# Kernel tuning notes

Measured on AMD Instinct MI355X. Metric: run time of the kernel, lower is better.

The kernel has to match this reference:

```python
import jax, jax.numpy as jnp
import numpy as np

H, C = 8, 16          # heads, per-head dim; hidden = H*C = 128
NEG_SLOPE = 0.2       # GATConv default
EPS = 1e-5            # GraphNorm eps


def setup_inputs() -> dict:
    key = jax.random.key(0)
    ks = iter(jax.random.split(key, 64))
    Np, Na, D, E = 100000, 50000, 128, 500000
    s = 1.0 / np.sqrt(D)

    def w(shape, scale=1.0):
        return jax.random.normal(next(ks), shape, jnp.float32) * scale

    inp = {
        'x_paper': w((Np, D)),
        'x_author': w((Na, D)),
        'edge_writes': jnp.stack([
            jax.random.randint(next(ks), (E,), 0, Na),
            jax.random.randint(next(ks), (E,), 0, Np)]).astype(jnp.int32),
        'edge_cites': jnp.stack([
            jax.random.randint(next(ks), (E,), 0, Np),
            jax.random.randint(next(ks), (E,), 0, Np)]).astype(jnp.int32),
        'W_lin_paper': w((D, 128), s), 'b_lin_paper': jnp.zeros((128,), jnp.float32),
        'W_lin_author': w((D, 128), s), 'b_lin_author': jnp.zeros((128,), jnp.float32),
        'Wsrc_writes': w((128, 128), s), 'Wdst_writes': w((128, 128), s),
        'atts_writes': w((H, C), 0.1), 'attd_writes': w((H, C), 0.1),
        'bias_writes': jnp.zeros((128,), jnp.float32),
        'Wsrc_cites': w((128, 128), s), 'Wdst_cites': w((128, 128), s),
        'atts_cites': w((H, C), 0.1), 'attd_cites': w((H, C), 0.1),
        'bias_cites': jnp.zeros((128,), jnp.float32),
        'gnw_paper': jnp.ones((128,), jnp.float32), 'gnb_paper': jnp.zeros((128,), jnp.float32),
        'gnm_paper': jnp.ones((128,), jnp.float32),
        'gnw_author': jnp.ones((128,), jnp.float32), 'gnb_author': jnp.zeros((128,), jnp.float32),
        'gnm_author': jnp.ones((128,), jnp.float32),
        'W2_paper': w((128, 128), s), 'b2_paper': jnp.zeros((128,), jnp.float32),
        'W2_author': w((128, 128), s), 'b2_author': jnp.zeros((128,), jnp.float32),
    }
    return inp


def _gat(src_emb, dst_emb, ei, Wsrc, Wdst, att_s, att_d, bias, n_dst):
    # PyG GATConv, bipartite input, concat=True, add_self_loops=True (eval / no dropout)
    n_self = min(src_emb.shape[0], n_dst)
    loops = jnp.arange(n_self, dtype=ei.dtype)
    src = jnp.concatenate([ei[0], loops])
    dst = jnp.concatenate([ei[1], loops])
    xs = (src_emb @ Wsrc).reshape(-1, H, C)          # [Ns,H,C]
    xd = (dst_emb @ Wdst).reshape(-1, H, C)          # [Nd,H,C]
    a_s = (xs * att_s).sum(-1)                       # [Ns,H]
    a_d = (xd * att_d).sum(-1)                       # [Nd,H]
    e = jax.nn.leaky_relu(a_s[src] + a_d[dst], NEG_SLOPE)   # [E,H]
    m = jax.ops.segment_max(e, dst, num_segments=n_dst)
    m = jnp.where(jnp.isfinite(m), m, 0.0)           # guard empty segments
    p = jnp.exp(e - m[dst])
    denom = jax.ops.segment_sum(p, dst, num_segments=n_dst)
    alpha = p / (denom[dst] + 1e-16)                 # segment softmax over dst
    msg = xs[src] * alpha[:, :, None]                # [E,H,C]
    out = jax.ops.segment_sum(msg, dst, num_segments=n_dst)  # [Nd,H,C]
    return out.reshape(n_dst, H * C) + bias


def _gnorm(x, w, b, ms):
    mu = x.mean(0)
    o = x - ms * mu
    var = (o * o).mean(0)
    return w * o * jax.lax.rsqrt(var + EPS) + b


def reference(x_paper, x_author, edge_writes, edge_cites,
              W_lin_paper, b_lin_paper, W_lin_author, b_lin_author,
              Wsrc_writes, Wdst_writes, atts_writes, attd_writes, bias_writes,
              Wsrc_cites, Wdst_cites, atts_cites, attd_cites, bias_cites,
              gnw_paper, gnb_paper, gnm_paper, gnw_author, gnb_author, gnm_author,
              W2_paper, b2_paper, W2_author, b2_author):
    emb_p = jax.nn.relu(x_paper @ W_lin_paper + b_lin_paper)
    emb_a = jax.nn.relu(x_author @ W_lin_author + b_lin_author)
    Np = emb_p.shape[0]
    out_p = _gat(emb_a, emb_p, edge_writes, Wsrc_writes, Wdst_writes,
                 atts_writes, attd_writes, bias_writes, Np)
    out_p = out_p + _gat(emb_p, emb_p, edge_cites, Wsrc_cites, Wdst_cites,
                         atts_cites, attd_cites, bias_cites, Np)
    out_a = jnp.zeros((emb_a.shape[0], H * C), x_author.dtype)  # no edge type targets author
    out_p = _gnorm(out_p, gnw_paper, gnb_paper, gnm_paper) @ W2_paper + b2_paper
    out_a = _gnorm(out_a, gnw_author, gnb_author, gnm_author) @ W2_author + b2_author
    return (out_p, out_a)
```

## Files before the change

kernel.cpp:

```cpp
#include <hip/hip_runtime.h>
#include <cstdint>
#include <cstddef>

#define H 8
#define DHID 128
#define BM 64
#define LDST 136
#define NEG_SLOPE 0.2f
#define GN_EPS 1e-5f

#define SCAN_T 256
#define SCAN_I 4

typedef __attribute__((ext_vector_type(8))) short short8;
typedef __attribute__((ext_vector_type(4))) float f32x4;

__device__ __forceinline__ void atomAddF(float* p, float v) {
    __hip_atomic_fetch_add(p, v, __ATOMIC_RELAXED, __HIP_MEMORY_SCOPE_AGENT);
}
__device__ __forceinline__ unsigned short f2bf(float f) {
    uint32_t u = __float_as_uint(f);
    uint32_t r = (u + 0x7FFFu + ((u >> 16) & 1u)) >> 16;
    return (unsigned short)r;
}
__device__ __forceinline__ uint32_t pack2bf(float lo, float hi) {
    return (uint32_t)f2bf(lo) | ((uint32_t)f2bf(hi) << 16);
}
__device__ __forceinline__ float bflo(uint32_t v) { return __uint_as_float(v << 16); }
__device__ __forceinline__ float bfhi(uint32_t v) { return __uint_as_float(v & 0xFFFF0000u); }

struct PrepHist {
    const float *Wlp, *Wsc, *Wla, *Wsw, *W2p;
    const float *Wdw, *adw, *asc_, *Wdc, *adc_, *asw_;
    unsigned short *WlinP_p, *WsrcP_c, *WlinP_a, *WsrcP_w, *W2P_p, *VscP_p, *VscP_a;
    const float *bw, *bc, *gnb_a, *W2a, *b2a;
    float *bsum, *row_a, *colsum, *colsumsq;
    unsigned short *xs_w_ph, *xs_c_ph;
    float *as_w_ph, *as_c_ph;
    const int *dst_w, *dst_c;
    int *deg, *rank;
    int Ew, nself_w, Ec, nself_c, Np, HB0;
};

__global__ void prep_hist(PrepHist a) {
    int b = blockIdx.x, t = threadIdx.x;
    if (b >= a.HB0) {
        int i = (b - a.HB0) * 256 + t;
        int tw = a.Ew + a.nself_w;
        if (i < tw) {
            int d = (i < a.Ew) ? a.dst_w[i] : (i - a.Ew);
            a.rank[i] = atomicAdd(&a.deg[d], 1);
        } else {
            int j = i - tw;
            if (j < a.Ec + a.nself_c) {
                int d = (j < a.Ec) ? a.dst_c[j] : (j - a.Ec);
                a.rank[i] = atomicAdd(&a.deg[a.Np + d], 1);
            }
        }
        return;
    }
    if (b == 56) {
        if (t < 128) {
            a.bsum[t] = a.bw[t] + a.bc[t];
            float acc = a.b2a[t];
            for (int k = 0; k < DHID; ++k) acc += a.gnb_a[k] * a.W2a[k * DHID + t];
            a.row_a[t] = acc;
            a.colsum[t] = 0.f;
            a.colsumsq[t] = 0.f;
            a.xs_w_ph[t] = 0;
            a.xs_c_ph[t] = 0;
        } else if (t < 136) a.as_w_ph[t - 128] = -1e30f;
        else if (t < 144) a.as_c_ph[t - 136] = -1e30f;
        return;
    }
    int j = b >> 3;
    int idx = (b & 7) * 256 + t;
    int lane = idx & 63, kk = (idx >> 6) & 3, nt = idx >> 8;
    int col = nt * 16 + (lane & 15);
    int k0 = kk * 32 + ((lane >> 4) << 3);
    if (j < 5) {
        const float* W = j == 0 ? a.Wlp : j == 1 ? a.Wsc : j == 2 ? a.Wla : j == 3 ? a.Wsw : a.W2p;
        unsigned short* out = j == 0 ? a.WlinP_p : j == 1 ? a.WsrcP_c : j == 2 ? a.WlinP_a
                              : j == 3 ? a.WsrcP_w : a.W2P_p;
        for (int i = 0; i < 8; ++i) out[idx * 8 + i] = f2bf(W[(k0 + i) * DHID + col]);
    } else if (j == 5) {
        if (idx >= 2 * 256) return;
        const float *W = nullptr, *A = nullptr;
        int h = col & 7;
        if (col < 24) {
            int which = col >> 3;
            W = which == 0 ? a.Wdw : which == 1 ? a.Wsc : a.Wdc;
            A = which == 0 ? a.adw : which == 1 ? a.asc_ : a.adc_;
        }
        for (int i = 0; i < 8; ++i) {
            float v = 0.f;
            if (W)
                for (int c = 0; c < 16; ++c) v += W[(k0 + i) * DHID + h * 16 + c] * A[h * 16 + c];
            a.VscP_p[idx * 8 + i] = f2bf(v);
        }
    } else {
        if (idx >= 256) return;
        int h = col & 7;
        for (int i = 0; i < 8; ++i) {
            float v = 0.f;
            if (col < 8)
                for (int c = 0; c < 16; ++c)
                    v += a.Wsw[(k0 + i) * DHID + h * 16 + c] * a.asw_[h * 16 + c];
            a.VscP_a[idx * 8 + i] = f2bf(v);
        }
    }
}

__global__ void scan1(const int* __restrict__ in, int n, int* __restrict__ out,
                      int* __restrict__ bsums) {
    __shared__ int sh[SCAN_T];
    int t = threadIdx.x;
    long base = (long)blockIdx.x * SCAN_T * SCAN_I;
    int v[SCAN_I];
    int s = 0;
#pragma unroll
    for (int j = 0; j < SCAN_I; ++j) {
        long idx = base + (long)t * SCAN_I + j;
        int x = (idx < n) ? in[idx] : 0;
        x = (x + 3) & ~3;
        v[j] = x;
        s += x;
    }
    sh[t] = s;
    __syncthreads();
    for (int off = 1; off < SCAN_T; off <<= 1) {
        int x = (t >= off) ? sh[t - off] : 0;
        __syncthreads();
        sh[t] += x;
        __syncthreads();
    }
    int run = sh[t] - s;
#pragma unroll
    for (int j = 0; j < SCAN_I; ++j) {
        long idx = base + (long)t * SCAN_I + j;
        if (idx < n) out[idx] = run;
        run += v[j];
    }
    if (t == SCAN_T - 1) bsums[blockIdx.x] = sh[SCAN_T - 1];
}

__global__ void scan3_prefill(const int* __restrict__ off_raw, const int* __restrict__ bs1,
                              int nb, int n2, int* __restrict__ off2,
                              int Np, int Na, int maxTot, int* __restrict__ srcu) {
    __shared__ int pf[SCAN_T];
    int t = threadIdx.x;
    pf[t] = (t < nb) ? bs1[t] : 0;
    __syncthreads();
    for (int off = 1; off < SCAN_T; off <<= 1) {
        int x = (t >= off) ? pf[t - off] : 0;
        __syncthreads();
        pf[t] += x;
        __syncthreads();
    }
    int i = blockIdx.x * 256 + t;
    if (i < n2) {
        int g = i >> 10;
        off2[i] = off_raw[i] + (g ? pf[g - 1] : 0);
    }
    if (blockIdx.x == 0 && t == 0) off2[n2] = pf[nb - 1];
    int gm = Np >> 10;
    int mid = off_raw[Np] + (gm ? pf[gm - 1] : 0);
    long stride = (long)gridDim.x * 256;
    for (long k = i; k < maxTot; k += stride) srcu[k] = (k < (long)mid) ? Na : Np;
}

template <int NSC>
__device__ void proj_body(unsigned short* xt, int bid,
                          const float* __restrict__ x, int nrows,
                          const unsigned short* __restrict__ WlinP, const float* __restrict__ blin,
                          const unsigned short* __restrict__ WsrcP,
                          const unsigned short* __restrict__ VscP,
                          unsigned short* __restrict__ xs,
                          float* __restrict__ a0, float* __restrict__ a1, float* __restrict__ a2) {
    int t = threadIdx.x;
    int lane = t & 63, w = t >> 6;
    long row0 = (long)bid * BM;
    for (int it = 0; it < 16; ++it) {
        int idx2 = t + it * 256;
        int r = idx2 >> 6, cp = idx2 & 63;
        long gr = row0 + r;
        float v0 = 0.f, v1 = 0.f;
        if (gr < nrows) { v0 = x[gr * DHID + 2 * cp]; v1 = x[gr * DHID + 2 * cp + 1]; }
        *reinterpret_cast<uint32_t*>(&xt[r * LDST + 2 * cp]) = pack2bf(v0, v1);
    }
    __syncthreads();
    int arow = w * 16 + (lane & 15);
    int koff = (lane >> 4) << 3;
    short8 af[4];
#pragma unroll
    for (int kk = 0; kk < 4; ++kk)
        af[kk] = *reinterpret_cast<const short8*>(&xt[arow * LDST + kk * 32 + koff]);
    const short8* Bl = reinterpret_cast<const short8*>(WlinP);
    f32x4 acc[8];
#pragma unroll
    for (int nt = 0; nt < 8; ++nt) {
        f32x4 a = {0.f, 0.f, 0.f, 0.f};
#pragma unroll
        for (int kk = 0; kk < 4; ++kk)
            a = __builtin_amdgcn_mfma_f32_16x16x32_bf16(af[kk], Bl[(nt * 4 + kk) * 64 + lane], a, 0, 0, 0);
        acc[nt] = a;
    }
    __syncthreads();
    int orow = w * 16 + ((lane >> 4) << 2);
    int ccol = lane & 15;
#pragma unroll
    for (int nt = 0; nt < 8; ++nt) {
        float b = blin[nt * 16 + ccol];
#pragma unroll
        for (int r = 0; r < 4; ++r) {
            float e = fmaxf(acc[nt][r] + b, 0.f);
            xt[(orow + r) * LDST + nt * 16 + ccol] = f2bf(e);
        }
    }
    __syncthreads();
#pragma unroll
    for (int kk = 0; kk < 4; ++kk)
        af[kk] = *reinterpret_cast<const short8*>(&xt[arow * LDST + kk * 32 + koff]);
    const short8* Bs = reinterpret_cast<const short8*>(WsrcP);
#pragma unroll
    for (int nt = 0; nt < 8; ++nt) {
        f32x4 a = {0.f, 0.f, 0.f, 0.f};
#pragma unroll
        for (int kk = 0; kk < 4; ++kk)
            a = __builtin_amdgcn_mfma_f32_16x16x32_bf16(af[kk], Bs[(nt * 4 + kk) * 64 + lane], a, 0, 0, 0);
        acc[nt] = a;
    }
    const short8* Bv = reinterpret_cast<const short8*>(VscP);
    f32x4 sacc0 = {0.f, 0.f, 0.f, 0.f}, sacc1 = {0.f, 0.f, 0.f, 0.f};
#pragma unroll
    for (int kk = 0; kk < 4; ++kk)
        sacc0 = __builtin_amdgcn_mfma_f32_16x16x32_bf16(af[kk], Bv[kk * 64 + lane], sacc0, 0, 0, 0);
    if (NSC > 1) {
#pragma unroll
        for (int kk = 0; kk < 4; ++kk)
            sacc1 = __builtin_amdgcn_mfma_f32_16x16x32_bf16(af[kk], Bv[(4 + kk) * 64 + lane], sacc1, 0, 0, 0);
    }
#pragma unroll
    for (int nt = 0; nt < 8; ++nt) {
#pragma unroll
        for (int r = 0; r < 4; ++r) {
            long gr = row0 + orow + r;
            if (gr < nrows) xs[gr * DHID + nt * 16 + ccol] = f2bf(acc[nt][r]);
        }
    }
#pragma unroll
    for (int st = 0; st < NSC; ++st) {
        int scol = st * 16 + ccol;
        int h = scol & 7, which = scol >> 3;
        float* ap = which == 0 ? a0 : which == 1 ? a1 : which == 2 ? a2 : nullptr;
        if (ap) {
            f32x4 s = st == 0 ? sacc0 : sacc1;
#pragma unroll
            for (int r = 0; r < 4; ++r) {
                long gr = row0 + orow + r;
                if (gr < nrows) ap[gr * H + h] = s[r];
            }
        }
    }
}

struct MegaArgs {
    const float* x_p; int Np;
    const unsigned short* WlinP_p; const float* blp;
    const unsigned short* WsrcP_c; const unsigned short* VscP_p;
    unsigned short* xs_c; float *a_d_w, *a_s_c, *a_d_c;
    const float* x_a; int Na;
    const unsigned short* WlinP_a; const float* bla;
    const unsigned short* WsrcP_w; const unsigned short* VscP_a;
    unsigned short* xs_w; float* a_s_w;
    const int *src_w, *dst_w, *src_c, *dst_c;
    int Ew, nself_w, Ec, nself_c;
    const int *off2, *rank;
    int* srcu;
    int PB, AB;
};

__global__ __launch_bounds__(256) void mega(MegaArgs a) {
    __shared__ unsigned short xt[BM * LDST];
    int b = blockIdx.x;
    if (b < a.PB) {
        proj_body<2>(xt, b, a.x_p, a.Np, a.WlinP_p, a.blp, a.WsrcP_c, a.VscP_p,
                     a.xs_c, a.a_d_w, a.a_s_c, a.a_d_c);
        return;
    }
    if (b < a.PB + a.AB) {
        proj_body<1>(xt, b - a.PB, a.x_a, a.Na, a.WlinP_a, a.bla, a.WsrcP_w, a.VscP_a,
                     a.xs_w, a.a_s_w, nullptr, nullptr);
        return;
    }
    int i = (b - a.PB - a.AB) * 256 + threadIdx.x;
    int tw = a.Ew + a.nself_w;
    int s, di;
    if (i < tw) {
        if (i < a.Ew) { s = a.src_w[i]; di = a.dst_w[i]; } else { s = di = i - a.Ew; }
    } else {
        int j = i - tw;
        if (j >= a.Ec + a.nself_c) return;
        if (j < a.Ec) { s = a.src_c[j]; di = a.Np + a.dst_c[j]; }
        else { s = j - a.Ec; di = a.Np + (j - a.Ec); }
    }
    a.srcu[a.off2[di] + a.rank[i]] = s;
}

__global__ __launch_bounds__(256) void gat_gather(
    const int* __restrict__ off, const int* __restrict__ srcu,
    const float* __restrict__ a_s_w, const float* __restrict__ a_d_w,
    const float* __restrict__ a_s_c, const float* __restrict__ a_d_c,
    const unsigned short* __restrict__ xs_w, const unsigned short* __restrict__ xs_c,
    uint32_t* __restrict__ gatb, int Np) {
    int l = threadIdx.x & 63;
    int d = blockIdx.x * 4 + (threadIdx.x >> 6);
    if (d >= Np) return;
    int h = l >> 3;
    int iw = off[d], w1 = off[d + 1];
    int ic = off[Np + d], c1 = off[Np + d + 1];
    float adw = a_d_w[(long)d * H + h];
    float adc = a_d_c[(long)d * H + h];
    float denw = 0.f, n0w = 0.f, n1w = 0.f;
    float denc = 0.f, n0c = 0.f, n1c = 0.f;
    while (iw < w1 || ic < c1) {
        bool hw = iw < w1, hc = ic < c1;
        int4 sw, sc;
        if (hw) sw = *reinterpret_cast<const int4*>(srcu + iw);
        if (hc) sc = *reinterpret_cast<const int4*>(srcu + ic);
        float ew[4], ec[4];
        uint32_t vw[4], vc[4];
        if (hw) {
            ew[0] = a_s_w[(long)sw.x * H + h];
            ew[1] = a_s_w[(long)sw.y * H + h];
            ew[2] = a_s_w[(long)sw.z * H + h];
            ew[3] = a_s_w[(long)sw.w * H + h];
            vw[0] = *reinterpret_cast<const uint32_t*>(xs_w + (long)sw.x * DHID + 2 * l);
            vw[1] = *reinterpret_cast<const uint32_t*>(xs_w + (long)sw.y * DHID + 2 * l);
            vw[2] = *reinterpret_cast<const uint32_t*>(xs_w + (long)sw.z * DHID + 2 * l);
            vw[3] = *reinterpret_cast<const uint32_t*>(xs_w + (long)sw.w * DHID + 2 * l);
        }
        if (hc) {
            ec[0] = a_s_c[(long)sc.x * H + h];
            ec[1] = a_s_c[(long)sc.y * H + h];
            ec[2] = a_s_c[(long)sc.z * H + h];
            ec[3] = a_s_c[(long)sc.w * H + h];
            vc[0] = *reinterpret_cast<const uint32_t*>(xs_c + (long)sc.x * DHID + 2 * l);
            vc[1] = *reinterpret_cast<const uint32_t*>(xs_c + (long)sc.y * DHID + 2 * l);
            vc[2] = *reinterpret_cast<const uint32_t*>(xs_c + (long)sc.z * DHID + 2 * l);
            vc[3] = *reinterpret_cast<const uint32_t*>(xs_c + (long)sc.w * DHID + 2 * l);
        }
        if (hw) {
#pragma unroll
            for (int j = 0; j < 4; ++j) {
                float e = ew[j] + adw;
                e = e > 0.f ? e : NEG_SLOPE * e;
                float p = __expf(e);
                denw += p;
                n0w += p * bflo(vw[j]);
                n1w += p * bfhi(vw[j]);
            }
            iw += 4;
        }
        if (hc) {
#pragma unroll
            for (int j = 0; j < 4; ++j) {
                float e = ec[j] + adc;
                e = e > 0.f ? e : NEG_SLOPE * e;
                float p = __expf(e);
                denc += p;
                n0c += p * bflo(vc[j]);
                n1c += p * bfhi(vc[j]);
            }
            ic += 4;
        }
    }
    float rw = 1.f / (denw + 1e-16f);
    float rc = 1.f / (denc + 1e-16f);
    gatb[(long)d * 64 + l] = pack2bf(n0w * rw + n0c * rc, n1w * rw + n1c * rc);
}

#define GN_ROWS 512
__global__ void gn_reduce(const uint32_t* __restrict__ gatb, const float* __restrict__ bsum,
                          float* __restrict__ colsum, float* __restrict__ colsumsq, int Np) {
    int t = threadIdx.x;
    int p = t & 63, ro = t >> 6;
    long r0 = (long)blockIdx.x * GN_ROWS + ro;
    long r1 = min((long)(blockIdx.x + 1) * GN_ROWS, (long)Np);
    float b0 = bsum[2 * p], b1 = bsum[2 * p + 1];
    float s1a = 0.f, s2a = 0.f, s1b = 0.f, s2b = 0.f;
    for (long r = r0; r < r1; r += 4) {
        uint32_t u = gatb[r * 64 + p];
        float x0 = bflo(u) + b0, x1 = bfhi(u) + b1;
        s1a += x0; s2a += x0 * x0;
        s1b += x1; s2b += x1 * x1;
    }
    atomAddF(colsum + 2 * p, s1a);
    atomAddF(colsumsq + 2 * p, s2a);
    atomAddF(colsum + 2 * p + 1, s1b);
    atomAddF(colsumsq + 2 * p + 1, s2b);
}

__global__ __launch_bounds__(256) void final_fill(
    const uint32_t* __restrict__ gatb, const float* __restrict__ bsum,
    const float* __restrict__ colsum, const float* __restrict__ colsumsq,
    const float* __restrict__ gnw, const float* __restrict__ gnb,
    const float* __restrict__ gnm,
    const unsigned short* __restrict__ W2P, const float* __restrict__ b2,
    float* __restrict__ out, int Np, int FB,
    const float* __restrict__ row_a, float4* __restrict__ outa, long n4) {
    __shared__ unsigned short xt[BM * LDST];
    __shared__ float cscale[DHID], cshift[DHID];
    int b = blockIdx.x;
    int t = threadIdx.x;
    if (b >= FB) {
        long i = (long)(b - FB) * 256 + t;
        long stride = (long)(gridDim.x - FB) * 256;
        const float4* r4 = reinterpret_cast<const float4*>(row_a);
        for (; i < n4; i += stride) outa[i] = r4[i & 31];
        return;
    }
    int lane = t & 63, w = t >> 6;
    long row0 = (long)b * BM;
    if (t < DHID) {
        float invN = 1.f / (float)Np;
        float mu = colsum[t] * invN;
        float ms = gnm[t];
        float var = colsumsq[t] * invN - mu * mu * ms * (2.f - ms);
        float sc = gnw[t] * rsqrtf(var + GN_EPS);
        cscale[t] = sc;
        cshift[t] = (bsum[t] - ms * mu) * sc + gnb[t];
    }
    __syncthreads();
    for (int it = 0; it < 16; ++it) {
        int idx2 = t + it * 256;
        int r = idx2 >> 6, cp = idx2 & 63;
        long gr = row0 + r;
        float v0 = 0.f, v1 = 0.f;
        if (gr < Np) {
            uint32_t u = gatb[gr * 64 + cp];
            v0 = bflo(u) * cscale[2 * cp] + cshift[2 * cp];
            v1 = bfhi(u) * cscale[2 * cp + 1] + cshift[2 * cp + 1];
        }
        *reinterpret_cast<uint32_t*>(&xt[r * LDST + 2 * cp]) = pack2bf(v0, v1);
    }
    __syncthreads();
    int arow = w * 16 + (lane & 15);
    int koff = (lane >> 4) << 3;
    short8 af[4];
#pragma unroll
    for (int kk = 0; kk < 4; ++kk)
        af[kk] = *reinterpret_cast<const short8*>(&xt[arow * LDST + kk * 32 + koff]);
    const short8* Bw = reinterpret_cast<const short8*>(W2P);
    int orow = w * 16 + ((lane >> 4) << 2);
    int ccol = lane & 15;
#pragma unroll
    for (int nt = 0; nt < 8; ++nt) {
        f32x4 a = {0.f, 0.f, 0.f, 0.f};
#pragma unroll
        for (int kk = 0; kk < 4; ++kk)
            a = __builtin_amdgcn_mfma_f32_16x16x32_bf16(af[kk], Bw[(nt * 4 + kk) * 64 + lane], a, 0, 0, 0);
        float bb = b2[nt * 16 + ccol];
#pragma unroll
        for (int r = 0; r < 4; ++r) {
            long gr = row0 + orow + r;
            if (gr < Np) out[gr * DHID + nt * 16 + ccol] = a[r] + bb;
        }
    }
}

extern "C" void kernel_launch(void* const* d_in, const int* in_sizes, int n_in,
                              void* d_out, int out_size, void* d_ws, size_t ws_size,
                              hipStream_t stream) {
    const float* x_p   = (const float*)d_in[0];
    const float* x_a   = (const float*)d_in[1];
    const int*   e_w   = (const int*)d_in[2];
    const int*   e_c   = (const int*)d_in[3];
    const float* Wlp   = (const float*)d_in[4];
    const float* blp   = (const float*)d_in[5];
    const float* Wla   = (const float*)d_in[6];
    const float* bla   = (const float*)d_in[7];
    const float* Wsw   = (const float*)d_in[8];
    const float* Wdw   = (const float*)d_in[9];
    const float* asw   = (const float*)d_in[10];
    const float* adw   = (const float*)d_in[11];
    const float* bw    = (const float*)d_in[12];
    const float* Wsc   = (const float*)d_in[13];
    const float* Wdc   = (const float*)d_in[14];
    const float* asc   = (const float*)d_in[15];
    const float* adc   = (const float*)d_in[16];
    const float* bc    = (const float*)d_in[17];
    const float* gnw_p = (const float*)d_in[18];
    const float* gnb_p = (const float*)d_in[19];
    const float* gnm_p = (const float*)d_in[20];
    const float* gnb_a = (const float*)d_in[22];
    const float* W2p   = (const float*)d_in[24];
    const float* b2p   = (const float*)d_in[25];
    const float* W2a   = (const float*)d_in[26];
    const float* b2a   = (const float*)d_in[27];

    int Np = in_sizes[0] / DHID;
    int Na = in_sizes[1] / DHID;
    int Ew = in_sizes[2] / 2;
    int Ec = in_sizes[3] / 2;
    int nself_w = Na < Np ? Na : Np;
    int nself_c = Np;
    int tot_all = (Ew + nself_w) + (Ec + nself_c);
    int maxTot = tot_all + 6 * Np + 8;

    float* ws = (float*)d_ws;
    uint32_t* gatb = (uint32_t*)ws;
    float* a_d_w = (float*)(gatb + (size_t)Np * 64);
    float* a_d_c = a_d_w + (size_t)Np * H;
    float* a_s_w = a_d_c + (size_t)Np * H;
    float* a_s_c = a_s_w + (size_t)(Na + 1) * H;
    float* bsum  = a_s_c + (size_t)(Np + 1) * H;
    float* row_a = bsum + DHID;
    float* colsum   = row_a + DHID;
    float* colsumsq = colsum + DHID;
    int*   deg   = (int*)(colsumsq + DHID);
    int* off_raw = deg + 2 * Np;
    int* off2    = off_raw + 2 * Np;
    int* bs1     = off2 + 2 * Np + 1;
    uintptr_t up = (uintptr_t)(bs1 + 512);
    up = (up + 15) & ~(uintptr_t)15;
    int* srcu = (int*)up;
    int* rank = srcu + maxTot;
    unsigned short* xs_w = (unsigned short*)(rank + tot_all);
    unsigned short* xs_c = xs_w + (size_t)(Na + 1) * DHID;
    up = (uintptr_t)(xs_c + (size_t)(Np + 1) * DHID);
    up = (up + 15) & ~(uintptr_t)15;
    unsigned short* WlinP_p = (unsigned short*)up;
    unsigned short* WsrcP_c = WlinP_p + 16384;
    unsigned short* WlinP_a = WsrcP_c + 16384;
    unsigned short* WsrcP_w = WlinP_a + 16384;
    unsigned short* W2P_p   = WsrcP_w + 16384;
    unsigned short* VscP_p  = W2P_p + 16384;
    unsigned short* VscP_a  = VscP_p + 4096;

    hipMemsetAsync(deg, 0, 2 * (size_t)Np * sizeof(int), stream);

    int HB = (tot_all + 255) / 256;
    {
        PrepHist pa;
        pa.Wlp = Wlp; pa.Wsc = Wsc; pa.Wla = Wla; pa.Wsw = Wsw; pa.W2p = W2p;
        pa.Wdw = Wdw; pa.adw = adw; pa.asc_ = asc; pa.Wdc = Wdc; pa.adc_ = adc; pa.asw_ = asw;
        pa.WlinP_p = WlinP_p; pa.WsrcP_c = WsrcP_c; pa.WlinP_a = WlinP_a;
        pa.WsrcP_w = WsrcP_w; pa.W2P_p = W2P_p; pa.VscP_p = VscP_p; pa.VscP_a = VscP_a;
        pa.bw = bw; pa.bc = bc; pa.gnb_a = gnb_a; pa.W2a = W2a; pa.b2a = b2a;
        pa.bsum = bsum; pa.row_a = row_a; pa.colsum = colsum; pa.colsumsq = colsumsq;
        pa.xs_w_ph = xs_w + (size_t)Na * DHID;
        pa.xs_c_ph = xs_c + (size_t)Np * DHID;
        pa.as_w_ph = a_s_w + (size_t)Na * H;
        pa.as_c_ph = a_s_c + (size_t)Np * H;
        pa.dst_w = e_w + Ew; pa.dst_c = e_c + Ec;
        pa.deg = deg; pa.rank = rank;
        pa.Ew = Ew; pa.nself_w = nself_w; pa.Ec = Ec; pa.nself_c = nself_c;
        pa.Np = Np; pa.HB0 = 57;
        prep_hist<<<57 + HB, 256, 0, stream>>>(pa);
    }

    int n2 = 2 * Np;
    int nb = (n2 + SCAN_T * SCAN_I - 1) / (SCAN_T * SCAN_I);
    scan1<<<nb, SCAN_T, 0, stream>>>(deg, n2, off_raw, bs1);

    scan3_prefill<<<(maxTot + 255) / 256, 256, 0, stream>>>(
        off_raw, bs1, nb, n2, off2, Np, Na, maxTot, srcu);

    {
        MegaArgs ma;
        ma.x_p = x_p; ma.Np = Np; ma.WlinP_p = WlinP_p; ma.blp = blp;
        ma.WsrcP_c = WsrcP_c; ma.VscP_p = VscP_p;
        ma.xs_c = xs_c; ma.a_d_w = a_d_w; ma.a_s_c = a_s_c; ma.a_d_c = a_d_c;
        ma.x_a = x_a; ma.Na = Na; ma.WlinP_a = WlinP_a; ma.bla = bla;
        ma.WsrcP_w = WsrcP_w; ma.VscP_a = VscP_a;
        ma.xs_w = xs_w; ma.a_s_w = a_s_w;
        ma.src_w = e_w; ma.dst_w = e_w + Ew; ma.src_c = e_c; ma.dst_c = e_c + Ec;
        ma.Ew = Ew; ma.nself_w = nself_w; ma.Ec = Ec; ma.nself_c = nself_c;
        ma.off2 = off2; ma.rank = rank; ma.srcu = srcu;
        ma.PB = (Np + BM - 1) / BM;
        ma.AB = (Na + BM - 1) / BM;
        int SB = (tot_all + 255) / 256;
        mega<<<ma.PB + ma.AB + SB, 256, 0, stream>>>(ma);
    }

    gat_gather<<<(Np + 3) / 4, 256, 0, stream>>>(off2, srcu,
                                                 a_s_w, a_d_w, a_s_c, a_d_c,
                                                 xs_w, xs_c, gatb, Np);

    gn_reduce<<<(Np + GN_ROWS - 1) / GN_ROWS, 256, 0, stream>>>(gatb, bsum, colsum, colsumsq, Np);

    {
        int FB = (Np + BM - 1) / BM;
        long n4 = (long)Na * DHID / 4;
        final_fill<<<FB + 391, 256, 0, stream>>>(
            gatb, bsum, colsum, colsumsq, gnw_p, gnb_p, gnm_p, W2P_p, b2p,
            (float*)d_out, Np, FB,
            row_a, (float4*)((float*)d_out + (size_t)Np * DHID), n4);
    }
}
```

Measured before the change: 305.4 us.

## Handle self-loops inline in gather and load projection input directly to registers

New measurement: 301.5 us. No clear change (-1.3%).

```diff
diff --git a/kernel.cpp b/kernel.cpp
--- a/kernel.cpp
+++ b/kernel.cpp
@@ -28,6 +28,14 @@
 }
 __device__ __forceinline__ float bflo(uint32_t v) { return __uint_as_float(v << 16); }
 __device__ __forceinline__ float bfhi(uint32_t v) { return __uint_as_float(v & 0xFFFF0000u); }
+
+__device__ __forceinline__ short8 frag_from_f32(const float* __restrict__ p) {
+    float4 a = *reinterpret_cast<const float4*>(p);
+    float4 b = *reinterpret_cast<const float4*>(p + 4);
+    uint32_t arr[4] = {pack2bf(a.x, a.y), pack2bf(a.z, a.w),
+                       pack2bf(b.x, b.y), pack2bf(b.z, b.w)};
+    return *reinterpret_cast<short8*>(arr);
+}
 
 struct PrepHist {
     const float *Wlp, *Wsc, *Wla, *Wsw, *W2p;
@@ -39,23 +47,19 @@
     float *as_w_ph, *as_c_ph;
     const int *dst_w, *dst_c;
     int *deg, *rank;
-    int Ew, nself_w, Ec, nself_c, Np, HB0;
+    int Ew, Ec, Np, HB0;
 };
 
 __global__ void prep_hist(PrepHist a) {
     int b = blockIdx.x, t = threadIdx.x;
     if (b >= a.HB0) {
         int i = (b - a.HB0) * 256 + t;
-        int tw = a.Ew + a.nself_w;
-        if (i < tw) {
-            int d = (i < a.Ew) ? a.dst_w[i] : (i - a.Ew);
+        if (i < a.Ew) {
+            int d = a.dst_w[i];
             a.rank[i] = atomicAdd(&a.deg[d], 1);
-        } else {
-            int j = i - tw;
-            if (j < a.Ec + a.nself_c) {
-                int d = (j < a.Ec) ? a.dst_c[j] : (j - a.Ec);
-                a.rank[i] = atomicAdd(&a.deg[a.Np + d], 1);
-            }
+        } else if (i < a.Ew + a.Ec) {
+            int d = a.dst_c[i - a.Ew];
+            a.rank[i] = atomicAdd(&a.deg[a.Np + d], 1);
         }
         return;
     }
@@ -180,21 +184,21 @@
     int t = threadIdx.x;
     int lane = t & 63, w = t >> 6;
     long row0 = (long)bid * BM;
-    for (int it = 0; it < 16; ++it) {
-        int idx2 = t + it * 256;
-        int r = idx2 >> 6, cp = idx2 & 63;
-        long gr = row0 + r;
-        float v0 = 0.f, v1 = 0.f;
-        if (gr < nrows) { v0 = x[gr * DHID + 2 * cp]; v1 = x[gr * DHID + 2 * cp + 1]; }
-        *reinterpret_cast<uint32_t*>(&xt[r * LDST + 2 * cp]) = pack2bf(v0, v1);
-    }
-    __syncthreads();
     int arow = w * 16 + (lane & 15);
     int koff = (lane >> 4) << 3;
+    long gra = row0 + arow;
     short8 af[4];
-#pragma unroll
-    for (int kk = 0; kk < 4; ++kk)
-        af[kk] = *reinterpret_cast<const short8*>(&xt[arow * LDST + kk * 32 + koff]);
+    if (gra < nrows) {
+#pragma unroll
+        for (int kk = 0; kk < 4; ++kk)
+            af[kk] = frag_from_f32(x + gra * DHID + kk * 32 + koff);
+    } else {
+#pragma unroll
+        for (int kk = 0; kk < 4; ++kk) {
+#pragma unroll
+            for (int i = 0; i < 8; ++i) af[kk][i] = 0;
+        }
+    }
     const short8* Bl = reinterpret_cast<const short8*>(WlinP);
     f32x4 acc[8];
 #pragma unroll
@@ -205,7 +209,6 @@
             a = __builtin_amdgcn_mfma_f32_16x16x32_bf16(af[kk], Bl[(nt * 4 + kk) * 64 + lane], a, 0, 0, 0);
         acc[nt] = a;
     }
-    __syncthreads();
     int orow = w * 16 + ((lane >> 4) << 2);
     int ccol = lane & 15;
 #pragma unroll
@@ -274,7 +277,7 @@
     const unsigned short* WsrcP_w; const unsigned short* VscP_a;
     unsigned short* xs_w; float* a_s_w;
     const int *src_w, *dst_w, *src_c, *dst_c;
-    int Ew, nself_w, Ec, nself_c;
+    int Ew, Ec;
     const int *off2, *rank;
     int* srcu;
     int PB, AB;
@@ -294,16 +297,10 @@
         return;
     }
     int i = (b - a.PB - a.AB) * 256 + threadIdx.x;
-    int tw = a.Ew + a.nself_w;
     int s, di;
-    if (i < tw) {
-        if (i < a.Ew) { s = a.src_w[i]; di = a.dst_w[i]; } else { s = di = i - a.Ew; }
-    } else {
-        int j = i - tw;
-        if (j >= a.Ec + a.nself_c) return;
-        if (j < a.Ec) { s = a.src_c[j]; di = a.Np + a.dst_c[j]; }
-        else { s = j - a.Ec; di = a.Np + (j - a.Ec); }
-    }
+    if (i < a.Ew) { s = a.src_w[i]; di = a.dst_w[i]; }
+    else if (i < a.Ew + a.Ec) { int j = i - a.Ew; s = a.src_c[j]; di = a.Np + a.dst_c[j]; }
+    else return;
     a.srcu[a.off2[di] + a.rank[i]] = s;
 }
 
@@ -312,7 +309,7 @@
     const float* __restrict__ a_s_w, const float* __restrict__ a_d_w,
     const float* __restrict__ a_s_c, const float* __restrict__ a_d_c,
     const unsigned short* __restrict__ xs_w, const unsigned short* __restrict__ xs_c,
-    uint32_t* __restrict__ gatb, int Np) {
+    uint32_t* __restrict__ gatb, int Np, int nselfw) {
     int l = threadIdx.x & 63;
     int d = blockIdx.x * 4 + (threadIdx.x >> 6);
     if (d >= Np) return;
@@ -323,6 +320,20 @@
     float adc = a_d_c[(long)d * H + h];
     float denw = 0.f, n0w = 0.f, n1w = 0.f;
     float denc = 0.f, n0c = 0.f, n1c = 0.f;
+    if (d < nselfw) {
+        float e = a_s_w[(long)d * H + h] + adw;
+        e = e > 0.f ? e : NEG_SLOPE * e;
+        float p = __expf(e);
+        uint32_t v = *reinterpret_cast<const uint32_t*>(xs_w + (long)d * DHID + 2 * l);
+        denw += p; n0w += p * bflo(v); n1w += p * bfhi(v);
+    }
+    {
+        float e = a_s_c[(long)d * H + h] + adc;
+        e = e > 0.f ? e : NEG_SLOPE * e;
+        float p = __expf(e);
+        uint32_t v = *reinterpret_cast<const uint32_t*>(xs_c + (long)d * DHID + 2 * l);
+        denc += p; n0c += p * bflo(v); n1c += p * bfhi(v);
+    }
     while (iw < w1 || ic < c1) {
         bool hw = iw < w1, hc = ic < c1;
         int4 sw, sc;
@@ -504,9 +515,8 @@
     int Ew = in_sizes[2] / 2;
     int Ec = in_sizes[3] / 2;
     int nself_w = Na < Np ? Na : Np;
-    int nself_c = Np;
-    int tot_all = (Ew + nself_w) + (Ec + nself_c);
-    int maxTot = tot_all + 6 * Np + 8;
+    int tot_edges = Ew + Ec;
+    int maxTot = tot_edges + 6 * Np + 8;
 
     float* ws = (float*)d_ws;
     uint32_t* gatb = (uint32_t*)ws;
@@ -526,7 +536,7 @@
     up = (up + 15) & ~(uintptr_t)15;
     int* srcu = (int*)up;
     int* rank = srcu + maxTot;
-    unsigned short* xs_w = (unsigned short*)(rank + tot_all);
+    unsigned short* xs_w = (unsigned short*)(rank + tot_edges);
     unsigned short* xs_c = xs_w + (size_t)(Na + 1) * DHID;
     up = (uintptr_t)(xs_c + (size_t)(Np + 1) * DHID);
     up = (up + 15) & ~(uintptr_t)15;
@@ -540,7 +550,7 @@
 
     hipMemsetAsync(deg, 0, 2 * (size_t)Np * sizeof(int), stream);
 
-    int HB = (tot_all + 255) / 256;
+    int HB = (tot_edges + 255) / 256;
     {
         PrepHist pa;
         pa.Wlp = Wlp; pa.Wsc = Wsc; pa.Wla = Wla; pa.Wsw = Wsw; pa.W2p = W2p;
@@ -555,7 +565,7 @@
         pa.as_c_ph = a_s_c + (size_t)Np * H;
         pa.dst_w = e_w + Ew; pa.dst_c = e_c + Ec;
         pa.deg = deg; pa.rank = rank;
-        pa.Ew = Ew; pa.nself_w = nself_w; pa.Ec = Ec; pa.nself_c = nself_c;
+        pa.Ew = Ew; pa.Ec = Ec;
         pa.Np = Np; pa.HB0 = 57;
         prep_hist<<<57 + HB, 256, 0, stream>>>(pa);
     }
@@ -576,17 +586,17 @@
         ma.WsrcP_w = WsrcP_w; ma.VscP_a = VscP_a;
         ma.xs_w = xs_w; ma.a_s_w = a_s_w;
         ma.src_w = e_w; ma.dst_w = e_w + Ew; ma.src_c = e_c; ma.dst_c = e_c + Ec;
-        ma.Ew = Ew; ma.nself_w = nself_w; ma.Ec = Ec; ma.nself_c = nself_c;
+        ma.Ew = Ew; ma.Ec = Ec;
         ma.off2 = off2; ma.rank = rank; ma.srcu = srcu;
         ma.PB = (Np + BM - 1) / BM;
         ma.AB = (Na + BM - 1) / BM;
-        int SB = (tot_all + 255) / 256;
+        int SB = (tot_edges + 255) / 256;
         mega<<<ma.PB + ma.AB + SB, 256, 0, stream>>>(ma);
     }
 
     gat_gather<<<(Np + 3) / 4, 256, 0, stream>>>(off2, srcu,
                                                  a_s_w, a_d_w, a_s_c, a_d_c,
-                                                 xs_w, xs_c, gatb, Np);
+                                                 xs_w, xs_c, gatb, Np, nself_w);
 
     gn_reduce<<<(Np + GN_ROWS - 1) / GN_ROWS, 256, 0, stream>>>(gatb, bsum, colsum, colsumsq, Np);
 
```
